# Optimization experiments

Measured on AMD Instinct MI355X. Metric: run time of the kernel, lower is better.

## Reference

```python
import jax, jax.numpy as jnp
import numpy as np

ALPHA = 1.0 / 10.0  # dt / tau

def setup_inputs() -> dict:
    key = jax.random.key(0)
    ks = jax.random.split(key, 5)
    seq_len, batch, input_dim, hidden = 256, 128, 256, 1024
    return {
        "input": jax.random.normal(ks[0], (seq_len, batch, input_dim), dtype=jnp.float32),
        "W_in": jax.random.normal(ks[1], (hidden, input_dim), dtype=jnp.float32) / np.sqrt(input_dim),
        "b_in": jax.random.normal(ks[2], (hidden,), dtype=jnp.float32) * 0.01,
        "W_hh": jax.random.normal(ks[3], (hidden, hidden), dtype=jnp.float32) / np.sqrt(hidden),
        "b_hh": jax.random.normal(ks[4], (hidden,), dtype=jnp.float32) * 0.01,
        "h0": jnp.zeros((hidden,), dtype=jnp.float32),
    }

def reference(input, W_in, b_in, W_hh, b_hh, h0):
    # input: [T, B, I] -> states: [T, B, H]
    # Precompute input projections for all timesteps (linear, same math as per-step).
    x_proj = jnp.einsum('tbi,hi->tbh', input, W_in) + b_in  # [T, B, H]
    h_init = jnp.broadcast_to(h0, (input.shape[1], h0.shape[0]))  # [B, H]

    def step(h, xp):
        rec = h @ W_hh.T + b_hh                       # [B, H]
        h_new = (1.0 - ALPHA) * h + ALPHA * (rec + xp)  # leaky integration (noise sigma = 0)
        h_new = jax.nn.relu(h_new)
        return h_new, h_new

    _, states = jax.lax.scan(step, h_init, x_proj)
    return states  # [T, B, H]
```

## Files before the change

kernel.cpp:

```cpp
#include <hip/hip_runtime.h>
#include <hip/hip_bf16.h>

#define T_LEN 256
#define B_DIM 128
#define I_DIM 256
#define H_DIM 1024

typedef __attribute__((ext_vector_type(8))) short short8;
typedef __attribute__((ext_vector_type(4))) float f32x4;

__device__ unsigned g_sync[256];

static __device__ __forceinline__ unsigned short f2bf(float f) {
  unsigned u = __float_as_uint(f);
  return (unsigned short)((u + 0x7fffu + ((u >> 16) & 1u)) >> 16);
}
static __device__ __forceinline__ float bf2f(unsigned short h) {
  return __uint_as_float((unsigned)h << 16);
}

__global__ __launch_bounds__(256) void xproj_gemm(
    const float* __restrict__ A, const float* __restrict__ W,
    const float* __restrict__ bias, float* __restrict__ C) {
  __shared__ float As[64][33];
  __shared__ float Ws[64][33];

  const int tid = threadIdx.x;
  const int m0 = blockIdx.y * 64;
  const int n0 = blockIdx.x * 64;
  const int ty = tid >> 4;
  const int tx = tid & 15;
  const int r   = tid >> 3;
  const int c4  = (tid & 7) << 2;

  float acc[4][4] = {};

  for (int kc = 0; kc < I_DIM; kc += 32) {
#pragma unroll
    for (int p = 0; p < 2; ++p) {
      const int rr = r + p * 32;
      const float4 a = *(const float4*)(A + (size_t)(m0 + rr) * I_DIM + kc + c4);
      As[rr][c4 + 0] = a.x; As[rr][c4 + 1] = a.y;
      As[rr][c4 + 2] = a.z; As[rr][c4 + 3] = a.w;
      const float4 w = *(const float4*)(W + (size_t)(n0 + rr) * I_DIM + kc + c4);
      Ws[rr][c4 + 0] = w.x; Ws[rr][c4 + 1] = w.y;
      Ws[rr][c4 + 2] = w.z; Ws[rr][c4 + 3] = w.w;
    }
    __syncthreads();
#pragma unroll
    for (int k = 0; k < 32; ++k) {
      float av[4], wv[4];
#pragma unroll
      for (int i = 0; i < 4; ++i) av[i] = As[ty * 4 + i][k];
#pragma unroll
      for (int j = 0; j < 4; ++j) wv[j] = Ws[tx * 4 + j][k];
#pragma unroll
      for (int i = 0; i < 4; ++i)
#pragma unroll
        for (int j = 0; j < 4; ++j)
          acc[i][j] = fmaf(av[i], wv[j], acc[i][j]);
    }
    __syncthreads();
  }

  const float4 bv = *(const float4*)(bias + n0 + tx * 4);
#pragma unroll
  for (int i = 0; i < 4; ++i) {
    float4 o;
    o.x = acc[i][0] + bv.x;
    o.y = acc[i][1] + bv.y;
    o.z = acc[i][2] + bv.z;
    o.w = acc[i][3] + bv.w;
    *(float4*)(C + (size_t)(m0 + ty * 4 + i) * H_DIM + n0 + tx * 4) = o;
  }
}

__global__ __launch_bounds__(256) void cvt_hi_lo(
    const float* __restrict__ X, unsigned short* __restrict__ Xh,
    unsigned short* __restrict__ Xl) {
  const int i4 = blockIdx.x * 256 + threadIdx.x;
  const float4 x = ((const float4*)X)[i4];
  ushort4 h, l;
  h.x = f2bf(x.x); l.x = f2bf(x.x - bf2f(h.x));
  h.y = f2bf(x.y); l.y = f2bf(x.y - bf2f(h.y));
  h.z = f2bf(x.z); l.z = f2bf(x.z - bf2f(h.z));
  h.w = f2bf(x.w); l.w = f2bf(x.w - bf2f(h.w));
  ((ushort4*)Xh)[i4] = h;
  ((ushort4*)Xl)[i4] = l;
}

__global__ __launch_bounds__(256) void xproj_mfma(
    const unsigned short* __restrict__ Ah, const unsigned short* __restrict__ Al,
    const unsigned short* __restrict__ Wh, const unsigned short* __restrict__ Wl,
    const float* __restrict__ bias, float* __restrict__ C) {
  const int tid  = threadIdx.x;
  const int wv   = tid >> 6;
  const int lane = tid & 63;
  const int ln   = lane & 15;
  const int q    = lane >> 4;
  const int mw   = wv >> 1;
  const int nw   = wv & 1;
  const int m0   = blockIdx.y * 128 + mw * 64;
  const int n0   = blockIdx.x * 64  + nw * 32;

  f32x4 acc[4][2] = {};

#pragma unroll
  for (int kc = 0; kc < 8; ++kc) {
    const int ko = kc * 32 + q * 8;
    short8 afh[4], afl[4], wfh[2], wfl[2];
#pragma unroll
    for (int fm = 0; fm < 4; ++fm) {
      const size_t off = (size_t)(m0 + fm * 16 + ln) * I_DIM + ko;
      afh[fm] = *(const short8*)(Ah + off);
      afl[fm] = *(const short8*)(Al + off);
    }
#pragma unroll
    for (int fn = 0; fn < 2; ++fn) {
      const size_t off = (size_t)(n0 + fn * 16 + ln) * I_DIM + ko;
      wfh[fn] = *(const short8*)(Wh + off);
      wfl[fn] = *(const short8*)(Wl + off);
    }
#pragma unroll
    for (int fm = 0; fm < 4; ++fm)
#pragma unroll
      for (int fn = 0; fn < 2; ++fn) {
        acc[fm][fn] = __builtin_amdgcn_mfma_f32_16x16x32_bf16(afh[fm], wfh[fn], acc[fm][fn], 0, 0, 0);
        acc[fm][fn] = __builtin_amdgcn_mfma_f32_16x16x32_bf16(afh[fm], wfl[fn], acc[fm][fn], 0, 0, 0);
        acc[fm][fn] = __builtin_amdgcn_mfma_f32_16x16x32_bf16(afl[fm], wfh[fn], acc[fm][fn], 0, 0, 0);
      }
  }

#pragma unroll
  for (int fn = 0; fn < 2; ++fn) {
    const int j = n0 + fn * 16 + ln;
    const float bj = bias[j];
#pragma unroll
    for (int fm = 0; fm < 4; ++fm)
#pragma unroll
      for (int r = 0; r < 4; ++r)
        C[(size_t)(m0 + fm * 16 + q * 4 + r) * H_DIM + j] = acc[fm][fn][r] + bj;
  }
}

__global__ __launch_bounds__(256) void cvt_w_bf16(
    const float* __restrict__ W, unsigned short* __restrict__ Wb) {
  const int i4 = blockIdx.x * 256 + threadIdx.x;
  const float4 w = ((const float4*)W)[i4];
  ushort4 o;
  o.x = f2bf(w.x); o.y = f2bf(w.y); o.z = f2bf(w.z); o.w = f2bf(w.w);
  ((ushort4*)Wb)[i4] = o;
}

__global__ __launch_bounds__(256) void init_hT0(
    const float* __restrict__ h0, unsigned short* __restrict__ hT) {
  const int idx = blockIdx.x * 256 + threadIdx.x;
  hT[idx] = f2bf(h0[idx & (H_DIM - 1)]);
  if (blockIdx.x == 0) g_sync[threadIdx.x] = 0u;
}

__global__ __launch_bounds__(256, 1) void rnn_persist(
    unsigned short* __restrict__ hT,
    const unsigned short* __restrict__ Wb,
    const float* __restrict__ b_hh,
    const float* __restrict__ h0,
    float* __restrict__ out)
{
  __shared__ short8 w_lds[2 * 2 * 16 * 64];
  __shared__ float red[2][2][16][33];

  const int tid  = threadIdx.x;
  const int wv   = tid >> 6;
  const int lane = tid & 63;
  const int ln   = lane & 15;
  const int q    = lane >> 4;

  const int bid = blockIdx.x;
  const int bq  = bid >> 5;
  const int lj  = bid & 31;
  const int j0  = lj * 32;
  const int mt  = wv & 1;
  const int kh  = wv >> 1;
  const int b0  = bq * 32 + mt * 16;

  {
    const int kh_f = wv >> 1, jf_f = wv & 1;
    const short8* __restrict__ src =
        (const short8*)(Wb + (size_t)(j0 + jf_f * 16 + ln) * H_DIM + kh_f * 512 + q * 8);
    short8* dst = &w_lds[((kh_f * 2 + jf_f) * 16) * 64 + lane];
#pragma unroll
    for (int kc = 0; kc < 16; ++kc) dst[kc * 64] = src[kc * 4];
  }

  const size_t HT = (size_t)B_DIM * H_DIM;
  const size_t arow = (size_t)(b0 + ln) * H_DIM + kh * 512 + q * 8;
  const unsigned short* __restrict__ ha0 = hT + arow;
  const unsigned short* __restrict__ ha1 = hT + HT + arow;

  float bj[2];
#pragma unroll
  for (int jf = 0; jf < 2; ++jf) bj[jf] = b_hh[j0 + jf * 16 + ln];

  const size_t obase = (size_t)(b0 + q * 4) * H_DIM + j0 + ln;

  float hcur[2][4];
#pragma unroll
  for (int jf = 0; jf < 2; ++jf) {
    const float h0j = h0[j0 + jf * 16 + ln];
#pragma unroll
    for (int r = 0; r < 4; ++r) hcur[jf][r] = h0j;
  }

  unsigned* pollp  = &g_sync[bq * 64 + kh * 32 + ((lane & 15) << 1) + mt];
  unsigned* myflag = &g_sync[bq * 64 + (lj << 1) + mt];

  float xcur[2][4];
  if (wv < 2) {
#pragma unroll
    for (int jf = 0; jf < 2; ++jf)
#pragma unroll
      for (int r = 0; r < 4; ++r)
        xcur[jf][r] = out[obase + (size_t)r * H_DIM + jf * 16];
  }
  asm volatile("s_waitcnt vmcnt(0)" ::: "memory");
  __syncthreads();

  for (int t = 0; t < T_LEN; ++t) {
    if (t > 0) {
      const unsigned tgt = (unsigned)t;
      for (;;) {
        unsigned fv;
        asm volatile("global_load_dword %0, %1, off sc0 sc1\n\t"
                     "s_waitcnt vmcnt(0)"
                     : "=v"(fv) : "v"(pollp) : "memory");
        if (__all((int)fv >= (int)tgt)) break;
        __builtin_amdgcn_s_sleep(2);
      }
    }
    __builtin_amdgcn_sched_barrier(0);

    const unsigned short* __restrict__ ha = (t & 1) ? ha1 : ha0;
    short8 hfrag[16];
#pragma unroll
    for (int kc = 0; kc < 16; ++kc) {
      asm volatile("global_load_dwordx4 %0, %1, off offset:%2 sc0 sc1"
                   : "=&v"(hfrag[kc]) : "v"(ha), "i"(kc * 64));
    }

    float xnext[2][4];
    if (wv < 2) {
      const int tn = (t + 1 < T_LEN) ? t + 1 : T_LEN - 1;
      const float* __restrict__ xnp = out + (size_t)tn * HT;
#pragma unroll
      for (int jf = 0; jf < 2; ++jf)
#pragma unroll
        for (int r = 0; r < 4; ++r) {
          const float* p = xnp + obase + (size_t)r * H_DIM + jf * 16;
          asm volatile("global_load_dword %0, %1, off"
                       : "=&v"(xnext[jf][r]) : "v"(p));
        }
      asm volatile("s_waitcnt vmcnt(8)" ::: "memory");
    } else {
      asm volatile("s_waitcnt vmcnt(0)" ::: "memory");
    }
    __builtin_amdgcn_sched_barrier(0);

    f32x4 a0[2], a1[2];
#pragma unroll
    for (int jf = 0; jf < 2; ++jf) { a0[jf] = (f32x4){0,0,0,0}; a1[jf] = (f32x4){0,0,0,0}; }
#pragma unroll
    for (int kc = 0; kc < 16; kc += 2) {
#pragma unroll
      for (int jf = 0; jf < 2; ++jf) {
        const short8 w0 = w_lds[((kh * 2 + jf) * 16 + kc) * 64 + lane];
        const short8 w1 = w_lds[((kh * 2 + jf) * 16 + kc + 1) * 64 + lane];
        a0[jf] = __builtin_amdgcn_mfma_f32_16x16x32_bf16(hfrag[kc],     w0, a0[jf], 0, 0, 0);
        a1[jf] = __builtin_amdgcn_mfma_f32_16x16x32_bf16(hfrag[kc + 1], w1, a1[jf], 0, 0, 0);
      }
    }
    f32x4 acc[2];
#pragma unroll
    for (int jf = 0; jf < 2; ++jf) acc[jf] = a0[jf] + a1[jf];

    if (wv >= 2) {
#pragma unroll
      for (int jf = 0; jf < 2; ++jf)
#pragma unroll
        for (int r = 0; r < 4; ++r)
          red[t & 1][mt][q * 4 + r][jf * 16 + ln] = acc[jf][r];
    }
    __syncthreads();
    if (wv < 2) {
      unsigned short* __restrict__ hnext = hT + (size_t)((t + 1) & 1) * HT;
      float* __restrict__ xio_t = out + (size_t)t * HT;
      float v[2][4];
#pragma unroll
      for (int jf = 0; jf < 2; ++jf)
#pragma unroll
        for (int r = 0; r < 4; ++r) {
          const float rec = acc[jf][r] + red[t & 1][mt][q * 4 + r][jf * 16 + ln];
          float x = 0.9f * hcur[jf][r] + 0.1f * (rec + bj[jf] + xcur[jf][r]);
          x = x > 0.f ? x : 0.f;
          v[jf][r] = x;
          hcur[jf][r] = x;
          __hip_atomic_store(&hnext[obase + (size_t)r * H_DIM + jf * 16],
                             f2bf(x), __ATOMIC_RELAXED, __HIP_MEMORY_SCOPE_AGENT);
        }
      asm volatile("s_waitcnt vmcnt(0)" ::: "memory");
      __builtin_amdgcn_sched_barrier(0);
      if ((tid & 63) == 0)
        __hip_atomic_store(myflag, (unsigned)(t + 1), __ATOMIC_RELAXED,
                           __HIP_MEMORY_SCOPE_AGENT);
#pragma unroll
      for (int jf = 0; jf < 2; ++jf)
#pragma unroll
        for (int r = 0; r < 4; ++r)
          xio_t[obase + (size_t)r * H_DIM + jf * 16] = v[jf][r];
#pragma unroll
      for (int jf = 0; jf < 2; ++jf)
#pragma unroll
        for (int r = 0; r < 4; ++r) xcur[jf][r] = xnext[jf][r];
    }
  }
}

extern "C" void kernel_launch(void* const* d_in, const int* in_sizes, int n_in,
                              void* d_out, int out_size, void* d_ws, size_t ws_size,
                              hipStream_t stream) {
  const float* input = (const float*)d_in[0];
  const float* W_in  = (const float*)d_in[1];
  const float* b_in  = (const float*)d_in[2];
  const float* W_hh  = (const float*)d_in[3];
  const float* b_hh  = (const float*)d_in[4];
  const float* h0    = (const float*)d_in[5];
  float* out = (float*)d_out;

  char* ws = (char*)d_ws;
  unsigned short* Wb  = (unsigned short*)ws;
  unsigned short* hT  = (unsigned short*)(ws + (2u << 20));
  unsigned short* Wih = (unsigned short*)(ws + (5u << 19));
  unsigned short* Wil = (unsigned short*)(ws + (3u << 20));
  unsigned short* Ah  = (unsigned short*)(ws + (4u << 20));
  unsigned short* Al  = (unsigned short*)(ws + (20u << 20));

  cvt_w_bf16<<<(H_DIM * H_DIM / 4) / 256, 256, 0, stream>>>(W_hh, Wb);
  init_hT0<<<(B_DIM * H_DIM) / 256, 256, 0, stream>>>(h0, hT);

  if (ws_size >= (36u << 20)) {
    cvt_hi_lo<<<(T_LEN * B_DIM * I_DIM / 4) / 256, 256, 0, stream>>>(input, Ah, Al);
    cvt_hi_lo<<<(H_DIM * I_DIM / 4) / 256, 256, 0, stream>>>(W_in, Wih, Wil);
    dim3 g1(H_DIM / 64, (T_LEN * B_DIM) / 128);
    xproj_mfma<<<g1, 256, 0, stream>>>(Ah, Al, Wih, Wil, b_in, out);
  } else {
    dim3 g1(H_DIM / 64, (T_LEN * B_DIM) / 64);
    xproj_gemm<<<g1, 256, 0, stream>>>(input, W_in, b_in, out);
  }

  {
    unsigned short* hT_ = hT;
    const unsigned short* Wb_ = Wb;
    const float* bhh_ = b_hh;
    const float* h0_ = h0;
    float* out_ = out;
    void* pargs[5] = {(void*)&hT_, (void*)&Wb_, (void*)&bhh_, (void*)&h0_, (void*)&out_};
    hipLaunchCooperativeKernel((const void*)rnn_persist, dim3(128), dim3(256),
                               pargs, 0, stream);
  }
}
```

Baseline: 1.936 ms.

## Split K across four waves with register-resident W_hh fragments

```diff
diff --git a/kernel.cpp b/kernel.cpp
--- a/kernel.cpp
+++ b/kernel.cpp
@@ -166,11 +166,10 @@
     const float* __restrict__ h0,
     float* __restrict__ out)
 {
-  __shared__ short8 w_lds[2 * 2 * 16 * 64];
-  __shared__ float red[2][2][16][33];
+  __shared__ float red[2][3][2][16][33];
 
   const int tid  = threadIdx.x;
-  const int wv   = tid >> 6;
+  const int kq   = tid >> 6;
   const int lane = tid & 63;
   const int ln   = lane & 15;
   const int q    = lane >> 4;
@@ -179,53 +178,50 @@
   const int bq  = bid >> 5;
   const int lj  = bid & 31;
   const int j0  = lj * 32;
-  const int mt  = wv & 1;
-  const int kh  = wv >> 1;
-  const int b0  = bq * 32 + mt * 16;
-
-  {
-    const int kh_f = wv >> 1, jf_f = wv & 1;
-    const short8* __restrict__ src =
-        (const short8*)(Wb + (size_t)(j0 + jf_f * 16 + ln) * H_DIM + kh_f * 512 + q * 8);
-    short8* dst = &w_lds[((kh_f * 2 + jf_f) * 16) * 64 + lane];
-#pragma unroll
-    for (int kc = 0; kc < 16; ++kc) dst[kc * 64] = src[kc * 4];
+  const int mt  = kq;
+
+  short8 wfrag[2][8];
+#pragma unroll
+  for (int jf = 0; jf < 2; ++jf) {
+    const short8* wp = (const short8*)(Wb + (size_t)(j0 + jf * 16 + ln) * H_DIM
+                                       + kq * 256 + q * 8);
+#pragma unroll
+    for (int kc = 0; kc < 8; ++kc) wfrag[jf][kc] = wp[kc * 4];
   }
 
   const size_t HT = (size_t)B_DIM * H_DIM;
-  const size_t arow = (size_t)(b0 + ln) * H_DIM + kh * 512 + q * 8;
-  const unsigned short* __restrict__ ha0 = hT + arow;
-  const unsigned short* __restrict__ ha1 = hT + HT + arow;
-
-  float bj[2];
-#pragma unroll
-  for (int jf = 0; jf < 2; ++jf) bj[jf] = b_hh[j0 + jf * 16 + ln];
-
-  const size_t obase = (size_t)(b0 + q * 4) * H_DIM + j0 + ln;
-
-  float hcur[2][4];
-#pragma unroll
-  for (int jf = 0; jf < 2; ++jf) {
-    const float h0j = h0[j0 + jf * 16 + ln];
-#pragma unroll
-    for (int r = 0; r < 4; ++r) hcur[jf][r] = h0j;
-  }
-
-  unsigned* pollp  = &g_sync[bq * 64 + kh * 32 + ((lane & 15) << 1) + mt];
-  unsigned* myflag = &g_sync[bq * 64 + (lj << 1) + mt];
-
-  float xcur[2][4];
-  if (wv < 2) {
+  const size_t o_m0 = (size_t)(bq * 32 + ln) * H_DIM + kq * 256 + q * 8;
+  const size_t o_m1 = o_m0 + (size_t)16 * H_DIM;
+
+  const bool epi = (kq < 2);
+  float bj2[2], hcur[2][4], xcur[2][4];
+  size_t obase = 0;
+  if (epi) {
+    obase = (size_t)(bq * 32 + mt * 16 + q * 4) * H_DIM + j0 + ln;
+#pragma unroll
+    for (int jf = 0; jf < 2; ++jf) {
+      bj2[jf] = b_hh[j0 + jf * 16 + ln];
+      const float h0j = h0[j0 + jf * 16 + ln];
+#pragma unroll
+      for (int r = 0; r < 4; ++r) {
+        hcur[jf][r] = h0j;
+        xcur[jf][r] = out[obase + (size_t)r * H_DIM + jf * 16];
+      }
+    }
+  }
+
+  unsigned* pollp  = &g_sync[bq * 64 + kq * 16 + ln];
+  unsigned* myflag = &g_sync[bq * 64 + lj * 2 + mt];
+
+  asm volatile("s_waitcnt vmcnt(0)" ::: "memory");
+
+  for (int t = 0; t < T_LEN; ++t) {
+    const int par = t & 1;
 #pragma unroll
     for (int jf = 0; jf < 2; ++jf)
 #pragma unroll
-      for (int r = 0; r < 4; ++r)
-        xcur[jf][r] = out[obase + (size_t)r * H_DIM + jf * 16];
-  }
-  asm volatile("s_waitcnt vmcnt(0)" ::: "memory");
-  __syncthreads();
-
-  for (int t = 0; t < T_LEN; ++t) {
+      for (int kc = 0; kc < 8; ++kc) asm volatile("" : "+v"(wfrag[jf][kc]));
+
     if (t > 0) {
       const unsigned tgt = (unsigned)t;
       for (;;) {
@@ -234,30 +230,35 @@
                      "s_waitcnt vmcnt(0)"
                      : "=v"(fv) : "v"(pollp) : "memory");
         if (__all((int)fv >= (int)tgt)) break;
-        __builtin_amdgcn_s_sleep(2);
+        __builtin_amdgcn_s_sleep(1);
       }
     }
     __builtin_amdgcn_sched_barrier(0);
 
-    const unsigned short* __restrict__ ha = (t & 1) ? ha1 : ha0;
-    short8 hfrag[16];
-#pragma unroll
-    for (int kc = 0; kc < 16; ++kc) {
+    const unsigned short* hpar = hT + (size_t)par * HT;
+    const unsigned short* p0 = hpar + o_m0;
+    const unsigned short* p1 = hpar + o_m1;
+    short8 hfrag[2][8];
+#pragma unroll
+    for (int kc = 0; kc < 8; ++kc)
       asm volatile("global_load_dwordx4 %0, %1, off offset:%2 sc0 sc1"
-                   : "=&v"(hfrag[kc]) : "v"(ha), "i"(kc * 64));
-    }
-
-    float xnext[2][4];
-    if (wv < 2) {
-      const int tn = (t + 1 < T_LEN) ? t + 1 : T_LEN - 1;
-      const float* __restrict__ xnp = out + (size_t)tn * HT;
+                   : "=&v"(hfrag[0][kc]) : "v"(p0), "i"(kc * 64));
+#pragma unroll
+    for (int kc = 0; kc < 8; ++kc)
+      asm volatile("global_load_dwordx4 %0, %1, off offset:%2 sc0 sc1"
+                   : "=&v"(hfrag[1][kc]) : "v"(p1), "i"(kc * 64));
+
+    float xnf[2][4];
+    if (epi) {
+      const int tn = (t + 1 < T_LEN) ? t + 1 : t;
+      const float* xb = out + (size_t)tn * HT;
 #pragma unroll
       for (int jf = 0; jf < 2; ++jf)
 #pragma unroll
         for (int r = 0; r < 4; ++r) {
-          const float* p = xnp + obase + (size_t)r * H_DIM + jf * 16;
+          const float* p = xb + obase + (size_t)r * H_DIM + jf * 16;
           asm volatile("global_load_dword %0, %1, off"
-                       : "=&v"(xnext[jf][r]) : "v"(p));
+                       : "=&v"(xnf[jf][r]) : "v"(p));
         }
       asm volatile("s_waitcnt vmcnt(8)" ::: "memory");
     } else {
@@ -265,61 +266,77 @@
     }
     __builtin_amdgcn_sched_barrier(0);
 
-    f32x4 a0[2], a1[2];
-#pragma unroll
-    for (int jf = 0; jf < 2; ++jf) { a0[jf] = (f32x4){0,0,0,0}; a1[jf] = (f32x4){0,0,0,0}; }
-#pragma unroll
-    for (int kc = 0; kc < 16; kc += 2) {
-#pragma unroll
-      for (int jf = 0; jf < 2; ++jf) {
-        const short8 w0 = w_lds[((kh * 2 + jf) * 16 + kc) * 64 + lane];
-        const short8 w1 = w_lds[((kh * 2 + jf) * 16 + kc + 1) * 64 + lane];
-        a0[jf] = __builtin_amdgcn_mfma_f32_16x16x32_bf16(hfrag[kc],     w0, a0[jf], 0, 0, 0);
-        a1[jf] = __builtin_amdgcn_mfma_f32_16x16x32_bf16(hfrag[kc + 1], w1, a1[jf], 0, 0, 0);
-      }
-    }
-    f32x4 acc[2];
-#pragma unroll
-    for (int jf = 0; jf < 2; ++jf) acc[jf] = a0[jf] + a1[jf];
-
-    if (wv >= 2) {
+    f32x4 acc[2][2];
+#pragma unroll
+    for (int m = 0; m < 2; ++m)
+#pragma unroll
+      for (int jf = 0; jf < 2; ++jf) acc[m][jf] = (f32x4){0.f, 0.f, 0.f, 0.f};
+#pragma unroll
+    for (int kc = 0; kc < 8; ++kc)
+#pragma unroll
+      for (int m = 0; m < 2; ++m)
+#pragma unroll
+        for (int jf = 0; jf < 2; ++jf)
+          acc[m][jf] = __builtin_amdgcn_mfma_f32_16x16x32_bf16(
+              hfrag[m][kc], wfrag[jf][kc], acc[m][jf], 0, 0, 0);
+
+    if (kq == 0) {
 #pragma unroll
       for (int jf = 0; jf < 2; ++jf)
 #pragma unroll
         for (int r = 0; r < 4; ++r)
-          red[t & 1][mt][q * 4 + r][jf * 16 + ln] = acc[jf][r];
+          red[par][0][1][q * 4 + r][jf * 16 + ln] = acc[1][jf][r];
+    } else if (kq == 1) {
+#pragma unroll
+      for (int jf = 0; jf < 2; ++jf)
+#pragma unroll
+        for (int r = 0; r < 4; ++r)
+          red[par][0][0][q * 4 + r][jf * 16 + ln] = acc[0][jf][r];
+    } else {
+#pragma unroll
+      for (int m = 0; m < 2; ++m)
+#pragma unroll
+        for (int jf = 0; jf < 2; ++jf)
+#pragma unroll
+          for (int r = 0; r < 4; ++r)
+            red[par][kq - 1][m][q * 4 + r][jf * 16 + ln] = acc[m][jf][r];
     }
     __syncthreads();
-    if (wv < 2) {
-      unsigned short* __restrict__ hnext = hT + (size_t)((t + 1) & 1) * HT;
-      float* __restrict__ xio_t = out + (size_t)t * HT;
-      float v[2][4];
-#pragma unroll
-      for (int jf = 0; jf < 2; ++jf)
-#pragma unroll
-        for (int r = 0; r < 4; ++r) {
-          const float rec = acc[jf][r] + red[t & 1][mt][q * 4 + r][jf * 16 + ln];
-          float x = 0.9f * hcur[jf][r] + 0.1f * (rec + bj[jf] + xcur[jf][r]);
-          x = x > 0.f ? x : 0.f;
-          v[jf][r] = x;
-          hcur[jf][r] = x;
-          __hip_atomic_store(&hnext[obase + (size_t)r * H_DIM + jf * 16],
-                             f2bf(x), __ATOMIC_RELAXED, __HIP_MEMORY_SCOPE_AGENT);
-        }
-      asm volatile("s_waitcnt vmcnt(0)" ::: "memory");
-      __builtin_amdgcn_sched_barrier(0);
-      if ((tid & 63) == 0)
-        __hip_atomic_store(myflag, (unsigned)(t + 1), __ATOMIC_RELAXED,
-                           __HIP_MEMORY_SCOPE_AGENT);
-#pragma unroll
-      for (int jf = 0; jf < 2; ++jf)
-#pragma unroll
-        for (int r = 0; r < 4; ++r)
-          xio_t[obase + (size_t)r * H_DIM + jf * 16] = v[jf][r];
-#pragma unroll
-      for (int jf = 0; jf < 2; ++jf)
-#pragma unroll
-        for (int r = 0; r < 4; ++r) xcur[jf][r] = xnext[jf][r];
+
+    if (epi) {
+      unsigned short* hnext = hT + (size_t)((t + 1) & 1) * HT;
+      float* xio_t = out + (size_t)t * HT;
+      auto body = [&](const f32x4 (&am)[2]) {
+        float v[2][4];
+#pragma unroll
+        for (int jf = 0; jf < 2; ++jf)
+#pragma unroll
+          for (int r = 0; r < 4; ++r) {
+            const int bl = q * 4 + r, jl = jf * 16 + ln;
+            const float rec = am[jf][r] + red[par][0][mt][bl][jl]
+                            + red[par][1][mt][bl][jl] + red[par][2][mt][bl][jl];
+            float x = 0.9f * hcur[jf][r] + 0.1f * (rec + bj2[jf] + xcur[jf][r]);
+            x = x > 0.f ? x : 0.f;
+            v[jf][r] = x;
+            hcur[jf][r] = x;
+            __hip_atomic_store(&hnext[obase + (size_t)r * H_DIM + jf * 16],
+                               f2bf(x), __ATOMIC_RELAXED,
+                               __HIP_MEMORY_SCOPE_AGENT);
+          }
+        asm volatile("s_waitcnt vmcnt(0)" ::: "memory");
+        __builtin_amdgcn_sched_barrier(0);
+        if (lane == 0)
+          __hip_atomic_store(myflag, (unsigned)(t + 1), __ATOMIC_RELAXED,
+                             __HIP_MEMORY_SCOPE_AGENT);
+#pragma unroll
+        for (int jf = 0; jf < 2; ++jf)
+#pragma unroll
+          for (int r = 0; r < 4; ++r) {
+            xio_t[obase + (size_t)r * H_DIM + jf * 16] = v[jf][r];
+            xcur[jf][r] = xnf[jf][r];
+          }
+      };
+      if (kq == 0) body(acc[0]); else body(acc[1]);
     }
   }
 }
```

New measurement: 1.807 ms. 1.07x faster.
